# Performance work log

Hardware: AMD Instinct MI355X
Metric: run time of the kernel (lower is better)

## Reference

```python
import jax, jax.numpy as jnp
import numpy as np

LEAKY_SLOPE = 0.5  # hardcoded in HGCNConv(leaky=0.5)
N_LAYERS = 2


def _spmm(rows, cols, vals, X, num_segments):
    # y[s] = sum_{k: seg[k]==s} vals[k] * X[gather[k]]
    return jax.ops.segment_sum(vals[:, None] * X[rows], cols, num_segments=num_segments)


def setup_inputs() -> dict:
    key = jax.random.key(0)
    k1, k2, k3, k4 = jax.random.split(key, 4)
    N, E, NNZ, D = 150000, 100000, 2400000, 64
    n_users = 100000
    ego_embeddings = jax.random.normal(k1, (N, D), dtype=jnp.float32)
    adj_vals = jax.random.uniform(k2, (NNZ,), dtype=jnp.float32)
    adj_rows = jax.random.randint(k3, (NNZ,), 0, N, dtype=jnp.int32)
    adj_cols = jax.random.randint(k4, (NNZ,), 0, E, dtype=jnp.int32)
    return {
        "ego_embeddings": ego_embeddings,
        "adj_vals": adj_vals,
        "adj_rows": adj_rows,
        "adj_cols": adj_cols,
        "n_users": n_users,
        "n_nodes": N,
        "n_edges": E,
    }


def reference(ego_embeddings, adj_vals, adj_rows, adj_cols, n_users, n_nodes, n_edges):
    embs = ego_embeddings
    for _ in range(N_LAYERS):
        # adj.T @ embs : [E, D]
        h = _spmm(adj_rows, adj_cols, adj_vals, embs, n_edges)
        # adj @ h : [N, D]
        h = _spmm(adj_cols, adj_rows, adj_vals, h, n_nodes)
        embs = jax.nn.leaky_relu(h, negative_slope=LEAKY_SLOPE)
    user_all = embs[:n_users]
    item_all = embs[n_users:]
    return user_all, item_all
```

## Files before the change

kernel.cpp:

```cpp
#include <hip/hip_runtime.h>


constexpr int D = 64;
constexpr float SLOPE = 0.5f;
constexpr int NPART = 8;

struct Edge { int src; float val; };

__device__ __forceinline__ void unpack_edge(long long w, int& src, float& val) {
    src = (int)(unsigned)(w & 0xffffffffLL);
    val = __int_as_float((int)(unsigned)((unsigned long long)w >> 32));
}


__global__ __launch_bounds__(256) void hist_kernel(
    const int* __restrict__ rows, const int* __restrict__ cols,
    int* __restrict__ deg_n, int* __restrict__ deg_e, int nnz)
{
    int t = blockIdx.x * blockDim.x + threadIdx.x;
    if (t >= nnz) return;
    atomicAdd(&deg_n[rows[t]], 1);
    atomicAdd(&deg_e[cols[t]], 1);
}


__global__ __launch_bounds__(256) void scan_phase1(
    const int* __restrict__ deg, int* __restrict__ partials, int n)
{
    __shared__ int red[256];
    int tid = threadIdx.x;
    int base = blockIdx.x * 1024 + tid * 4;
    int s = 0;
    #pragma unroll
    for (int k = 0; k < 4; ++k) {
        int i = base + k;
        if (i < n) s += deg[i];
    }
    red[tid] = s;
    __syncthreads();
    for (int d = 128; d > 0; d >>= 1) {
        if (tid < d) red[tid] += red[tid + d];
        __syncthreads();
    }
    if (tid == 0) partials[blockIdx.x] = red[0];
}

__global__ __launch_bounds__(256) void scan_phase2(
    int* __restrict__ partials, int nb, int* __restrict__ off, int n)
{
    __shared__ int part[256];
    int tid = threadIdx.x;
    part[tid] = (tid < nb) ? partials[tid] : 0;
    __syncthreads();
    for (int d = 1; d < 256; d <<= 1) {
        int v = (tid >= d) ? part[tid - d] : 0;
        __syncthreads();
        part[tid] += v;
        __syncthreads();
    }
    if (tid < nb) partials[tid] = (tid == 0) ? 0 : part[tid - 1];
    if (tid == 255) off[n] = part[255];
}

__global__ __launch_bounds__(256) void scan_phase3(
    const int* __restrict__ deg, const int* __restrict__ partials,
    int* __restrict__ off, int* __restrict__ cur, int n)
{
    __shared__ int part[256];
    int tid = threadIdx.x;
    int base = blockIdx.x * 1024 + tid * 4;
    int d0 = 0, d1 = 0, d2 = 0, d3 = 0;
    if (base     < n) d0 = deg[base];
    if (base + 1 < n) d1 = deg[base + 1];
    if (base + 2 < n) d2 = deg[base + 2];
    if (base + 3 < n) d3 = deg[base + 3];
    part[tid] = d0 + d1 + d2 + d3;
    __syncthreads();
    for (int d = 1; d < 256; d <<= 1) {
        int v = (tid >= d) ? part[tid - d] : 0;
        __syncthreads();
        part[tid] += v;
        __syncthreads();
    }
    int p = ((tid == 0) ? 0 : part[tid - 1]) + partials[blockIdx.x];
    if (base     < n) { off[base]     = p; cur[base]     = p; p += d0; }
    if (base + 1 < n) { off[base + 1] = p; cur[base + 1] = p; p += d1; }
    if (base + 2 < n) { off[base + 2] = p; cur[base + 2] = p; p += d2; }
    if (base + 3 < n) { off[base + 3] = p; cur[base + 3] = p; }
}

__global__ __launch_bounds__(256) void fill_list_kernel(
    const int* __restrict__ key, const int* __restrict__ other,
    const float* __restrict__ vals,
    int* __restrict__ cur, Edge* __restrict__ edges,
    int nnz, int S)
{
    int part   = blockIdx.x & (NPART - 1);
    int chunk  = blockIdx.x >> 3;
    int nchunk = gridDim.x >> 3;
    int lo = part * S, hi = lo + S;

    for (int t = chunk * blockDim.x + threadIdx.x; t < nnz;
         t += nchunk * blockDim.x) {
        int k = __builtin_nontemporal_load(key + t);
        if (k >= lo && k < hi) {
            int   o = __builtin_nontemporal_load(other + t);
            float v = __builtin_nontemporal_load(vals + t);
            int p = atomicAdd(&cur[k], 1);
            Edge e; e.src = o; e.val = v;
            edges[p] = e;
        }
    }
}

__global__ __launch_bounds__(256) void spmm_gather(
    const int* __restrict__ off, const Edge* __restrict__ edges,
    const float* __restrict__ X, float* __restrict__ out,
    int nrows, int leaky)
{
    int wid = (blockIdx.x * blockDim.x + threadIdx.x) >> 6;
    if (wid >= nrows) return;
    int lane = threadIdx.x & 63;

    const long long* ew = reinterpret_cast<const long long*>(edges);

    int b = __builtin_nontemporal_load(off + wid);
    int e = __builtin_nontemporal_load(off + wid + 1);
    float acc = 0.f;
    int i = b;
    for (; i + 4 <= e; i += 4) {
        long long w0 = __builtin_nontemporal_load(ew + i);
        long long w1 = __builtin_nontemporal_load(ew + i + 1);
        long long w2 = __builtin_nontemporal_load(ew + i + 2);
        long long w3 = __builtin_nontemporal_load(ew + i + 3);
        int s0, s1, s2, s3; float v0, v1, v2, v3;
        unpack_edge(w0, s0, v0);
        unpack_edge(w1, s1, v1);
        unpack_edge(w2, s2, v2);
        unpack_edge(w3, s3, v3);
        float x0 = X[(size_t)s0 * D + lane];
        float x1 = X[(size_t)s1 * D + lane];
        float x2 = X[(size_t)s2 * D + lane];
        float x3 = X[(size_t)s3 * D + lane];
        acc += v0 * x0;
        acc += v1 * x1;
        acc += v2 * x2;
        acc += v3 * x3;
    }
    for (; i < e; ++i) {
        long long w0 = __builtin_nontemporal_load(ew + i);
        int s0; float v0;
        unpack_edge(w0, s0, v0);
        acc += v0 * X[(size_t)s0 * D + lane];
    }
    if (leaky) acc = acc >= 0.f ? acc : SLOPE * acc;
    out[(size_t)wid * D + lane] = acc;
}


extern "C" void kernel_launch(void* const* d_in, const int* in_sizes, int n_in,
                              void* d_out, int out_size, void* d_ws, size_t ws_size,
                              hipStream_t stream)
{
    const float* ego  = (const float*)d_in[0];
    const float* vals = (const float*)d_in[1];
    const int*   rows = (const int*)d_in[2];
    const int*   cols = (const int*)d_in[3];

    const int nnz = in_sizes[1];
    const int N   = out_size / D;
    const int E   = 100000;

    float* outf = (float*)d_out;

    auto align16 = [](size_t x) { return (x + 15) & ~(size_t)15; };
    size_t o = 0;
    size_t edges_e_off = o; o += align16((size_t)nnz * sizeof(Edge));
    size_t edges_n_off = o; o += align16((size_t)nnz * sizeof(Edge));
    size_t off_e_off   = o; o += align16((size_t)(E + 1) * sizeof(int));
    size_t off_n_off   = o; o += align16((size_t)(N + 1) * sizeof(int));
    size_t cur_e_off   = o; o += align16((size_t)E * sizeof(int));
    size_t cur_n_off   = o; o += align16((size_t)N * sizeof(int));
    size_t part_e_off  = o; o += align16(256 * sizeof(int));
    size_t part_n_off  = o; o += align16(256 * sizeof(int));
    size_t h_off       = o; o += align16((size_t)E * D * sizeof(float));
    size_t embs_off    = o; o += align16((size_t)N * D * sizeof(float));
    size_t need = o;

    char* ws = (char*)d_ws;

    if (ws_size >= need) {
        Edge*  edges_e = (Edge*)(ws + edges_e_off);
        Edge*  edges_n = (Edge*)(ws + edges_n_off);
        int*   off_e   = (int*)(ws + off_e_off);
        int*   off_n   = (int*)(ws + off_n_off);
        int*   cur_e   = (int*)(ws + cur_e_off);
        int*   cur_n   = (int*)(ws + cur_n_off);
        int*   part_e  = (int*)(ws + part_e_off);
        int*   part_n  = (int*)(ws + part_n_off);
        float* h       = (float*)(ws + h_off);
        float* embs    = (float*)(ws + embs_off);

        const int nb_edge = (nnz + 255) / 256;
        const int nb_sc_e = (E + 1023) / 1024;
        const int nb_sc_n = (N + 1023) / 1024;

        (void)hipMemsetAsync(cur_e, 0, (size_t)E * sizeof(int), stream);
        (void)hipMemsetAsync(cur_n, 0, (size_t)N * sizeof(int), stream);
        hist_kernel<<<nb_edge, 256, 0, stream>>>(rows, cols, cur_n, cur_e, nnz);

        scan_phase1<<<nb_sc_e, 256, 0, stream>>>(cur_e, part_e, E);
        scan_phase1<<<nb_sc_n, 256, 0, stream>>>(cur_n, part_n, N);
        scan_phase2<<<1, 256, 0, stream>>>(part_e, nb_sc_e, off_e, E);
        scan_phase2<<<1, 256, 0, stream>>>(part_n, nb_sc_n, off_n, N);
        scan_phase3<<<nb_sc_e, 256, 0, stream>>>(cur_e, part_e, off_e, cur_e, E);
        scan_phase3<<<nb_sc_n, 256, 0, stream>>>(cur_n, part_n, off_n, cur_n, N);

        const int SE = (E + NPART - 1) / NPART;
        const int SN = (N + NPART - 1) / NPART;
        fill_list_kernel<<<1024, 256, 0, stream>>>(cols, rows, vals,
                                                   cur_e, edges_e, nnz, SE);
        fill_list_kernel<<<1024, 256, 0, stream>>>(rows, cols, vals,
                                                   cur_n, edges_n, nnz, SN);

        const int nb_spmm_e = (E * 64 + 255) / 256;
        const int nb_spmm_n = (N * 64 + 255) / 256;

        const float* X = ego;
        for (int layer = 0; layer < 2; ++layer) {
            float* Y = (layer == 0) ? embs : outf;
            spmm_gather<<<nb_spmm_e, 256, 0, stream>>>(off_e, edges_e, X, h, E, 0);
            spmm_gather<<<nb_spmm_n, 256, 0, stream>>>(off_n, edges_n, h, Y, N, 1);
            X = Y;
        }
    } else {
        (void)hipMemsetAsync(outf, 0, (size_t)out_size * sizeof(float), stream);
    }
}
```

Baseline: 1.075 ms.

## Build CSR via two-level bucket sort with shared-memory atomics

Replaces the global-atomic histogram and the partitioned atomic fill with a two-level counting sort. Keys are binned into 128-key buckets using per-block shared-memory counts, the bins are scanned, edges are scattered into buckets, and each bucket is then locally sorted in shared memory to produce the CSR offsets and the packed edge list. This is meant to remove contended global atomics and the eight repeated passes over the input in the CSR build. In exchange it adds extra passes through scratch buffers that reuse the h region. The gather SpMM itself is unchanged.

New measurement: 914.6 us. 14.9% less time.

```diff
diff --git a/kernel.cpp b/kernel.cpp
--- a/kernel.cpp
+++ b/kernel.cpp
@@ -3,7 +3,9 @@
 
 constexpr int D = 64;
 constexpr float SLOPE = 0.5f;
-constexpr int NPART = 8;
+constexpr int NBLK  = 192;
+constexpr int BSH   = 7;
+constexpr int NBMAX = 1280;
 
 struct Edge { int src; float val; };
 
@@ -12,17 +14,21 @@
     val = __int_as_float((int)(unsigned)((unsigned long long)w >> 32));
 }
 
-
-__global__ __launch_bounds__(256) void hist_kernel(
-    const int* __restrict__ rows, const int* __restrict__ cols,
-    int* __restrict__ deg_n, int* __restrict__ deg_e, int nnz)
-{
-    int t = blockIdx.x * blockDim.x + threadIdx.x;
-    if (t >= nnz) return;
-    atomicAdd(&deg_n[rows[t]], 1);
-    atomicAdd(&deg_e[cols[t]], 1);
-}
-
+__global__ __launch_bounds__(256) void bin_count_kernel(
+    const int* __restrict__ key, int* __restrict__ cnt_flat, int nnz, int NB)
+{
+    __shared__ int cnt[NBMAX];
+    int tid = threadIdx.x, blk = blockIdx.x;
+    for (int b = tid; b < NB; b += 256) cnt[b] = 0;
+    __syncthreads();
+    for (int t = blk * 256 + tid; t < nnz; t += NBLK * 256) {
+        int k = __builtin_nontemporal_load(key + t);
+        atomicAdd(&cnt[k >> BSH], 1);
+    }
+    __syncthreads();
+    for (int b = tid; b < NB; b += 256)
+        cnt_flat[(size_t)b * NBLK + blk] = cnt[b];
+}
 
 __global__ __launch_bounds__(256) void scan_phase1(
     const int* __restrict__ deg, int* __restrict__ partials, int n)
@@ -46,7 +52,7 @@
 }
 
 __global__ __launch_bounds__(256) void scan_phase2(
-    int* __restrict__ partials, int nb, int* __restrict__ off, int n)
+    int* __restrict__ partials, int nb)
 {
     __shared__ int part[256];
     int tid = threadIdx.x;
@@ -59,12 +65,11 @@
         __syncthreads();
     }
     if (tid < nb) partials[tid] = (tid == 0) ? 0 : part[tid - 1];
-    if (tid == 255) off[n] = part[255];
 }
 
 __global__ __launch_bounds__(256) void scan_phase3(
     const int* __restrict__ deg, const int* __restrict__ partials,
-    int* __restrict__ off, int* __restrict__ cur, int n)
+    int* __restrict__ out, int n)
 {
     __shared__ int part[256];
     int tid = threadIdx.x;
@@ -83,46 +88,82 @@
         __syncthreads();
     }
     int p = ((tid == 0) ? 0 : part[tid - 1]) + partials[blockIdx.x];
-    if (base     < n) { off[base]     = p; cur[base]     = p; p += d0; }
-    if (base + 1 < n) { off[base + 1] = p; cur[base + 1] = p; p += d1; }
-    if (base + 2 < n) { off[base + 2] = p; cur[base + 2] = p; p += d2; }
-    if (base + 3 < n) { off[base + 3] = p; cur[base + 3] = p; }
-}
-
-__global__ __launch_bounds__(256) void fill_list_kernel(
+    if (base     < n) { out[base]     = p; p += d0; }
+    if (base + 1 < n) { out[base + 1] = p; p += d1; }
+    if (base + 2 < n) { out[base + 2] = p; p += d2; }
+    if (base + 3 < n) { out[base + 3] = p; }
+}
+
+__global__ __launch_bounds__(256) void bin_scatter_kernel(
     const int* __restrict__ key, const int* __restrict__ other,
-    const float* __restrict__ vals,
-    int* __restrict__ cur, Edge* __restrict__ edges,
-    int nnz, int S)
-{
-    int part   = blockIdx.x & (NPART - 1);
-    int chunk  = blockIdx.x >> 3;
-    int nchunk = gridDim.x >> 3;
-    int lo = part * S, hi = lo + S;
-
-    for (int t = chunk * blockDim.x + threadIdx.x; t < nnz;
-         t += nchunk * blockDim.x) {
-        int k = __builtin_nontemporal_load(key + t);
-        if (k >= lo && k < hi) {
-            int   o = __builtin_nontemporal_load(other + t);
-            float v = __builtin_nontemporal_load(vals + t);
-            int p = atomicAdd(&cur[k], 1);
-            Edge e; e.src = o; e.val = v;
-            edges[p] = e;
-        }
+    const float* __restrict__ vals, const int* __restrict__ base_flat,
+    int* __restrict__ bkey, long long* __restrict__ bedge, int nnz, int NB)
+{
+    __shared__ int cur[NBMAX];
+    int tid = threadIdx.x, blk = blockIdx.x;
+    for (int b = tid; b < NB; b += 256)
+        cur[b] = base_flat[(size_t)b * NBLK + blk];
+    __syncthreads();
+    for (int t = blk * 256 + tid; t < nnz; t += NBLK * 256) {
+        int   k = __builtin_nontemporal_load(key + t);
+        int   o = __builtin_nontemporal_load(other + t);
+        float v = __builtin_nontemporal_load(vals + t);
+        int p = atomicAdd(&cur[k >> BSH], 1);
+        bkey[p] = k;
+        long long w = (long long)((unsigned long long)(unsigned)o |
+                                  ((unsigned long long)__float_as_uint(v) << 32));
+        bedge[p] = w;
+    }
+}
+
+__global__ __launch_bounds__(256) void bucket_sort_kernel(
+    const int* __restrict__ bkey, const long long* __restrict__ bedge,
+    const int* __restrict__ base_flat,
+    long long* __restrict__ edges, int* __restrict__ off,
+    int nnz, int NB, int K)
+{
+    __shared__ int sc[128];
+    __shared__ int cur[128];
+    int b = blockIdx.x, tid = threadIdx.x;
+    int start = base_flat[(size_t)b * NBLK];
+    int end   = (b == NB - 1) ? nnz : base_flat[(size_t)(b + 1) * NBLK];
+    int k0 = b << BSH;
+    int nk = K - k0; if (nk > 128) nk = 128;
+
+    if (tid < 128) sc[tid] = 0;
+    __syncthreads();
+    for (int t = start + tid; t < end; t += 256)
+        atomicAdd(&sc[bkey[t] - k0], 1);
+    __syncthreads();
+    for (int d = 1; d < 128; d <<= 1) {
+        int add = (tid < 128 && tid >= d) ? sc[tid - d] : 0;
+        __syncthreads();
+        if (tid < 128) sc[tid] += add;
+        __syncthreads();
+    }
+    if (tid < 128) {
+        int loc = (tid == 0) ? 0 : sc[tid - 1];
+        if (tid < nk) off[k0 + tid] = start + loc;
+        cur[tid] = loc;
+    }
+    if (b == NB - 1 && tid == 0) off[K] = nnz;
+    __syncthreads();
+    for (int t = start + tid; t < end; t += 256) {
+        int k = bkey[t] - k0;
+        long long w = bedge[t];
+        int p = atomicAdd(&cur[k], 1);
+        edges[start + p] = w;
     }
 }
 
 __global__ __launch_bounds__(256) void spmm_gather(
-    const int* __restrict__ off, const Edge* __restrict__ edges,
+    const int* __restrict__ off, const long long* __restrict__ ew,
     const float* __restrict__ X, float* __restrict__ out,
     int nrows, int leaky)
 {
     int wid = (blockIdx.x * blockDim.x + threadIdx.x) >> 6;
     if (wid >= nrows) return;
     int lane = threadIdx.x & 63;
-
-    const long long* ew = reinterpret_cast<const long long*>(edges);
 
     int b = __builtin_nontemporal_load(off + wid);
     int e = __builtin_nontemporal_load(off + wid + 1);
@@ -173,67 +214,74 @@
 
     float* outf = (float*)d_out;
 
+    const int NB_E = (E + 127) >> BSH;
+    const int NB_N = (N + 127) >> BSH;
+    const int L_E  = NB_E * NBLK;
+    const int L_N  = NB_N * NBLK;
+
     auto align16 = [](size_t x) { return (x + 15) & ~(size_t)15; };
     size_t o = 0;
-    size_t edges_e_off = o; o += align16((size_t)nnz * sizeof(Edge));
-    size_t edges_n_off = o; o += align16((size_t)nnz * sizeof(Edge));
-    size_t off_e_off   = o; o += align16((size_t)(E + 1) * sizeof(int));
-    size_t off_n_off   = o; o += align16((size_t)(N + 1) * sizeof(int));
-    size_t cur_e_off   = o; o += align16((size_t)E * sizeof(int));
-    size_t cur_n_off   = o; o += align16((size_t)N * sizeof(int));
-    size_t part_e_off  = o; o += align16(256 * sizeof(int));
-    size_t part_n_off  = o; o += align16(256 * sizeof(int));
-    size_t h_off       = o; o += align16((size_t)E * D * sizeof(float));
-    size_t embs_off    = o; o += align16((size_t)N * D * sizeof(float));
+    size_t edges_e_off = o; o += align16((size_t)nnz * 8);
+    size_t edges_n_off = o; o += align16((size_t)nnz * 8);
+    size_t off_e_off   = o; o += align16((size_t)(E + 1) * 4);
+    size_t off_n_off   = o; o += align16((size_t)(N + 1) * 4);
+    size_t cnt_off     = o; o += align16((size_t)L_N * 4);
+    size_t base_off    = o; o += align16((size_t)L_N * 4);
+    size_t parts_off   = o; o += align16(256 * 4);
+    size_t h_off       = o; o += align16((size_t)E * D * 4);
+    size_t embs_off    = o; o += align16((size_t)N * D * 4);
     size_t need = o;
 
     char* ws = (char*)d_ws;
-
-    if (ws_size >= need) {
-        Edge*  edges_e = (Edge*)(ws + edges_e_off);
-        Edge*  edges_n = (Edge*)(ws + edges_n_off);
-        int*   off_e   = (int*)(ws + off_e_off);
-        int*   off_n   = (int*)(ws + off_n_off);
-        int*   cur_e   = (int*)(ws + cur_e_off);
-        int*   cur_n   = (int*)(ws + cur_n_off);
-        int*   part_e  = (int*)(ws + part_e_off);
-        int*   part_n  = (int*)(ws + part_n_off);
-        float* h       = (float*)(ws + h_off);
-        float* embs    = (float*)(ws + embs_off);
-
-        const int nb_edge = (nnz + 255) / 256;
-        const int nb_sc_e = (E + 1023) / 1024;
-        const int nb_sc_n = (N + 1023) / 1024;
-
-        (void)hipMemsetAsync(cur_e, 0, (size_t)E * sizeof(int), stream);
-        (void)hipMemsetAsync(cur_n, 0, (size_t)N * sizeof(int), stream);
-        hist_kernel<<<nb_edge, 256, 0, stream>>>(rows, cols, cur_n, cur_e, nnz);
-
-        scan_phase1<<<nb_sc_e, 256, 0, stream>>>(cur_e, part_e, E);
-        scan_phase1<<<nb_sc_n, 256, 0, stream>>>(cur_n, part_n, N);
-        scan_phase2<<<1, 256, 0, stream>>>(part_e, nb_sc_e, off_e, E);
-        scan_phase2<<<1, 256, 0, stream>>>(part_n, nb_sc_n, off_n, N);
-        scan_phase3<<<nb_sc_e, 256, 0, stream>>>(cur_e, part_e, off_e, cur_e, E);
-        scan_phase3<<<nb_sc_n, 256, 0, stream>>>(cur_n, part_n, off_n, cur_n, N);
-
-        const int SE = (E + NPART - 1) / NPART;
-        const int SN = (N + NPART - 1) / NPART;
-        fill_list_kernel<<<1024, 256, 0, stream>>>(cols, rows, vals,
-                                                   cur_e, edges_e, nnz, SE);
-        fill_list_kernel<<<1024, 256, 0, stream>>>(rows, cols, vals,
-                                                   cur_n, edges_n, nnz, SN);
-
-        const int nb_spmm_e = (E * 64 + 255) / 256;
-        const int nb_spmm_n = (N * 64 + 255) / 256;
-
-        const float* X = ego;
-        for (int layer = 0; layer < 2; ++layer) {
-            float* Y = (layer == 0) ? embs : outf;
-            spmm_gather<<<nb_spmm_e, 256, 0, stream>>>(off_e, edges_e, X, h, E, 0);
-            spmm_gather<<<nb_spmm_n, 256, 0, stream>>>(off_n, edges_n, h, Y, N, 1);
-            X = Y;
-        }
-    } else {
+    if (ws_size < need) {
         (void)hipMemsetAsync(outf, 0, (size_t)out_size * sizeof(float), stream);
-    }
-}
+        return;
+    }
+
+    long long* edges_e = (long long*)(ws + edges_e_off);
+    long long* edges_n = (long long*)(ws + edges_n_off);
+    int*   off_e   = (int*)(ws + off_e_off);
+    int*   off_n   = (int*)(ws + off_n_off);
+    int*   cnt     = (int*)(ws + cnt_off);
+    int*   basef   = (int*)(ws + base_off);
+    int*   parts   = (int*)(ws + parts_off);
+    float* h       = (float*)(ws + h_off);
+    float* embs    = (float*)(ws + embs_off);
+
+    int*       bkey  = (int*)(ws + h_off);
+    long long* bedge = (long long*)(ws + h_off + align16((size_t)nnz * 4));
+
+    {
+        const int G1 = (L_E + 1023) / 1024;
+        bin_count_kernel<<<NBLK, 256, 0, stream>>>(cols, cnt, nnz, NB_E);
+        scan_phase1<<<G1, 256, 0, stream>>>(cnt, parts, L_E);
+        scan_phase2<<<1, 256, 0, stream>>>(parts, G1);
+        scan_phase3<<<G1, 256, 0, stream>>>(cnt, parts, basef, L_E);
+        bin_scatter_kernel<<<NBLK, 256, 0, stream>>>(cols, rows, vals, basef,
+                                                     bkey, bedge, nnz, NB_E);
+        bucket_sort_kernel<<<NB_E, 256, 0, stream>>>(bkey, bedge, basef,
+                                                     edges_e, off_e, nnz, NB_E, E);
+    }
+    {
+        const int G1 = (L_N + 1023) / 1024;
+        bin_count_kernel<<<NBLK, 256, 0, stream>>>(rows, cnt, nnz, NB_N);
+        scan_phase1<<<G1, 256, 0, stream>>>(cnt, parts, L_N);
+        scan_phase2<<<1, 256, 0, stream>>>(parts, G1);
+        scan_phase3<<<G1, 256, 0, stream>>>(cnt, parts, basef, L_N);
+        bin_scatter_kernel<<<NBLK, 256, 0, stream>>>(rows, cols, vals, basef,
+                                                     bkey, bedge, nnz, NB_N);
+        bucket_sort_kernel<<<NB_N, 256, 0, stream>>>(bkey, bedge, basef,
+                                                     edges_n, off_n, nnz, NB_N, N);
+    }
+
+    const int nb_spmm_e = (E * 64 + 255) / 256;
+    const int nb_spmm_n = (N * 64 + 255) / 256;
+
+    const float* X = ego;
+    for (int layer = 0; layer < 2; ++layer) {
+        float* Y = (layer == 0) ? embs : outf;
+        spmm_gather<<<nb_spmm_e, 256, 0, stream>>>(off_e, edges_e, X, h, E, 0);
+        spmm_gather<<<nb_spmm_n, 256, 0, stream>>>(off_n, edges_n, h, Y, N, 1);
+        X = Y;
+    }
+}
```
